# Kernel tuning notes

Hardware: AMD Instinct MI355X
Metric: run time of the kernel (lower is better)

The kernel has to match this reference:

```python
import jax, jax.numpy as jnp
import numpy as np

NUM_CLASSES = 80
L_BOX, L_OBJ, L_CLS = 5.0, 1.0, 1.0


def setup_inputs() -> dict:
    key = jax.random.key(0)
    k0, k1, k2, k3, k4 = jax.random.split(key, 5)
    B, N = 32, 50
    C = 5 + NUM_CLASSES
    pred0 = jax.random.normal(k0, (B, C, 64, 64), dtype=jnp.float32)
    pred1 = jax.random.normal(k1, (B, C, 32, 32), dtype=jnp.float32)
    pred2 = jax.random.normal(k2, (B, C, 16, 16), dtype=jnp.float32)
    # normalized cxcywh in (0,1)
    boxes = jax.random.uniform(k3, (B, N, 4), dtype=jnp.float32, minval=0.01, maxval=0.99)
    labels = jax.random.randint(k4, (B, N), 0, NUM_CLASSES, dtype=jnp.int32)
    return {"pred0": pred0, "pred1": pred1, "pred2": pred2, "boxes": boxes, "labels": labels}


def _bce_with_logits_mean(x, t):
    # numerically stable BCEWithLogits, mean reduction
    return jnp.mean(jnp.maximum(x, 0.0) - x * t + jnp.log1p(jnp.exp(-jnp.abs(x))))


def _build_targets(boxes, labels, b, h, w):
    # boxes: [B,N,4] normalized cxcywh; labels: [B,N]
    B, N, _ = boxes.shape
    bi = jnp.repeat(jnp.arange(B), N)            # [B*N]
    bf = boxes.reshape(-1, 4)                    # [B*N,4]
    lf = labels.reshape(-1)                      # [B*N]
    gx = bf[:, 0] * w
    gy = bf[:, 1] * h
    gi = jnp.minimum(gx.astype(jnp.int32), w - 1)  # int() truncation; gx >= 0
    gj = jnp.minimum(gy.astype(jnp.int32), h - 1)
    obj_t = jnp.zeros((b, 1, h, w), jnp.float32).at[bi, 0, gj, gi].set(1.0)
    vals = jnp.stack([gx - gi, gy - gj, bf[:, 2], bf[:, 3]], axis=1)  # [B*N,4]
    ch4 = jnp.arange(4)
    box_t = jnp.zeros((b, 4, h, w), jnp.float32).at[
        bi[:, None], ch4[None, :], gj[:, None], gi[:, None]].set(vals)
    cls_t = jnp.zeros((b, NUM_CLASSES, h, w), jnp.float32).at[bi, lf, gj, gi].set(1.0)
    return box_t, obj_t, cls_t


def _scale_loss(pred, boxes, labels):
    b, _, h, w = pred.shape
    box_t, obj_t, cls_t = _build_targets(boxes, labels, b, h, w)
    pb = jnp.clip(pred[:, :4], -10.0, 10.0)
    po = jnp.clip(pred[:, 4:5], -10.0, 10.0)
    pc = jnp.clip(pred[:, 5:], -10.0, 10.0)
    box_loss = jnp.mean((pb - box_t) ** 2)
    obj_loss = _bce_with_logits_mean(po, obj_t)
    cls_loss = _bce_with_logits_mean(pc, cls_t)
    # torch code zeroes non-finite losses; clamped logits keep these finite,
    # mirrored with jnp.where for faithfulness
    box_loss = jnp.where(jnp.isfinite(box_loss), box_loss, 0.0)
    obj_loss = jnp.where(jnp.isfinite(obj_loss), obj_loss, 0.0)
    cls_loss = jnp.where(jnp.isfinite(cls_loss), cls_loss, 0.0)
    return L_BOX * box_loss + L_OBJ * obj_loss + L_CLS * cls_loss


def reference(pred0, pred1, pred2, boxes, labels):
    total = (_scale_loss(pred0, boxes, labels)
             + _scale_loss(pred1, boxes, labels)
             + _scale_loss(pred2, boxes, labels))
    return jnp.clip(total / 3.0, 0.0, 1000000.0)
```

## Files before the change

kernel.cpp:

```cpp
#include <hip/hip_runtime.h>
#include <math.h>

#define NCLS 80
#define BB   32
#define NBOX 50
#define CC   85

#define GRID1 2048
#define BLK1  256

__device__ __forceinline__ float clip10(float x) {
    return fminf(fmaxf(x, -10.f), 10.f);
}

__device__ __forceinline__ float bce0(float x) {
    return fmaxf(x, 0.f) + __logf(1.f + __expf(-fabsf(x)));
}

__global__ __launch_bounds__(BLK1) void base_kernel(
    const float* __restrict__ p0, const float* __restrict__ p1,
    const float* __restrict__ p2, double* __restrict__ partial)
{
    const int tid = blockIdx.x * BLK1 + threadIdx.x;
    const int nth = GRID1 * BLK1;
    const float* ps[3] = {p0, p1, p2};
    const int hw4s[3]  = {64*64/4, 32*32/4, 16*16/4};

    float part[9];
    #pragma unroll
    for (int s = 0; s < 3; ++s) {
        const float4* p = (const float4*)ps[s];
        const int hw4 = hw4s[s];
        const int n4  = BB * CC * hw4;
        float bx = 0.f, ob = 0.f, cl = 0.f;
        for (int i = tid; i < n4; i += nth) {
            float4 v = p[i];
            int c = (i / hw4) % CC;
            float a0 = clip10(v.x), a1 = clip10(v.y);
            float a2 = clip10(v.z), a3 = clip10(v.w);
            if (c < 4) {
                bx += a0*a0 + a1*a1 + a2*a2 + a3*a3;
            } else if (c == 4) {
                ob += bce0(a0) + bce0(a1) + bce0(a2) + bce0(a3);
            } else {
                cl += bce0(a0) + bce0(a1) + bce0(a2) + bce0(a3);
            }
        }
        part[3*s+0] = bx; part[3*s+1] = ob; part[3*s+2] = cl;
    }

    #pragma unroll
    for (int k = 0; k < 9; ++k) {
        float v = part[k];
        #pragma unroll
        for (int off = 32; off > 0; off >>= 1) v += __shfl_down(v, off);
        part[k] = v;
    }
    __shared__ float sred[BLK1/64][9];
    const int wave = threadIdx.x >> 6;
    const int lane = threadIdx.x & 63;
    if (lane == 0) {
        #pragma unroll
        for (int k = 0; k < 9; ++k) sred[wave][k] = part[k];
    }
    __syncthreads();
    if (threadIdx.x == 0) {
        double* o = partial + (size_t)blockIdx.x * 9;
        #pragma unroll
        for (int k = 0; k < 9; ++k)
            o[k] = (double)(sred[0][k] + sred[1][k] + sred[2][k] + sred[3][k]);
    }
}

__global__ __launch_bounds__(64) void corr_kernel(
    const float* __restrict__ p0, const float* __restrict__ p1,
    const float* __restrict__ p2,
    const float* __restrict__ boxes, const int* __restrict__ labels,
    double* __restrict__ acc)
{
    const int s = blockIdx.x / BB;
    const int b = blockIdx.x % BB;
    const float* ps[3] = {p0, p1, p2};
    const int Ws[3] = {64, 32, 16};
    const int W = Ws[s], H = W, hw = W * W;
    const float* pred = ps[s];

    __shared__ int   s_cell[NBOX];
    __shared__ int   s_lab[NBOX];
    __shared__ float s_vx[NBOX], s_vy[NBOX], s_vw[NBOX], s_vh[NBOX];

    const int n = threadIdx.x;
    if (n < NBOX) {
        const float* bp = boxes + ((size_t)b * NBOX + n) * 4;
        float gx = bp[0] * (float)W;
        float gy = bp[1] * (float)H;
        int gi = min((int)gx, W - 1);
        int gj = min((int)gy, H - 1);
        s_cell[n] = gj * W + gi;
        s_lab[n]  = labels[b * NBOX + n];
        s_vx[n] = gx - (float)gi;
        s_vy[n] = gy - (float)gj;
        s_vw[n] = bp[2];
        s_vh[n] = bp[3];
    }
    __syncthreads();

    float cbx = 0.f, cob = 0.f, ccl = 0.f;
    if (n < NBOX) {
        const int cell = s_cell[n], lab = s_lab[n];
        bool lastCell = true, lastCls = true;
        for (int m = n + 1; m < NBOX; ++m) {
            if (s_cell[m] == cell) {
                lastCell = false;
                if (s_lab[m] == lab) lastCls = false;
            }
        }
        const float* pb_base = pred + (size_t)(b * CC) * hw + cell;
        if (lastCell) {
            float vals[4] = {s_vx[n], s_vy[n], s_vw[n], s_vh[n]};
            #pragma unroll
            for (int c = 0; c < 4; ++c) {
                float pb = clip10(pb_base[c * hw]);
                float d  = pb - vals[c];
                cbx += d * d - pb * pb;
            }
            float po = clip10(pb_base[4 * hw]);
            cob -= po;
        }
        if (lastCls) {
            float pc = clip10(pb_base[(5 + lab) * hw]);
            ccl -= pc;
        }
    }
    #pragma unroll
    for (int off = 32; off > 0; off >>= 1) {
        cbx += __shfl_down(cbx, off);
        cob += __shfl_down(cob, off);
        ccl += __shfl_down(ccl, off);
    }
    if (threadIdx.x == 0) {
        atomicAdd(&acc[3*s+0], (double)cbx);
        atomicAdd(&acc[3*s+1], (double)cob);
        atomicAdd(&acc[3*s+2], (double)ccl);
    }
}

__global__ __launch_bounds__(256) void final_kernel(
    const double* __restrict__ partial, const double* __restrict__ acc,
    float* __restrict__ out, int nb)
{
    double loc[9];
    #pragma unroll
    for (int k = 0; k < 9; ++k) loc[k] = 0.0;
    for (int i = threadIdx.x; i < nb; i += 256) {
        const double* row = partial + (size_t)i * 9;
        #pragma unroll
        for (int k = 0; k < 9; ++k) loc[k] += row[k];
    }
    __shared__ double sd[256];
    __shared__ double tot[9];
    for (int k = 0; k < 9; ++k) {
        sd[threadIdx.x] = loc[k];
        __syncthreads();
        for (int off = 128; off > 0; off >>= 1) {
            if (threadIdx.x < off) sd[threadIdx.x] += sd[threadIdx.x + off];
            __syncthreads();
        }
        if (threadIdx.x == 0) tot[k] = sd[0] + acc[k];
        __syncthreads();
    }
    if (threadIdx.x == 0) {
        const double hws[3] = {4096.0, 1024.0, 256.0};
        double total = 0.0;
        for (int s = 0; s < 3; ++s) {
            double hw  = hws[s];
            double box = tot[3*s+0] / (32.0 * 4.0 * hw);
            double ob  = tot[3*s+1] / (32.0 * hw);
            double cl  = tot[3*s+2] / (32.0 * 80.0 * hw);
            total += 5.0 * box + ob + cl;
        }
        total /= 3.0;
        total = fmin(fmax(total, 0.0), 1000000.0);
        out[0] = (float)total;
    }
}

extern "C" void kernel_launch(void* const* d_in, const int* in_sizes, int n_in,
                              void* d_out, int out_size, void* d_ws, size_t ws_size,
                              hipStream_t stream)
{
    const float* p0     = (const float*)d_in[0];
    const float* p1     = (const float*)d_in[1];
    const float* p2     = (const float*)d_in[2];
    const float* boxes  = (const float*)d_in[3];
    const int*   labels = (const int*)d_in[4];
    float* out = (float*)d_out;

    double* acc     = (double*)d_ws;
    double* partial = (double*)d_ws + 16;

    hipMemsetAsync(acc, 0, 9 * sizeof(double), stream);
    base_kernel<<<GRID1, BLK1, 0, stream>>>(p0, p1, p2, partial);
    corr_kernel<<<3 * BB, 64, 0, stream>>>(p0, p1, p2, boxes, labels, acc);
    final_kernel<<<1, 256, 0, stream>>>(partial, acc, out, GRID1);
}
```

Baseline: 119.9 us.

## Fold target-correction pass into base reduction kernel and drop memset

Result: faster. 102.5 us (-14.5%).

```diff
diff --git a/kernel.cpp b/kernel.cpp
--- a/kernel.cpp
+++ b/kernel.cpp
@@ -19,7 +19,9 @@
 
 __global__ __launch_bounds__(BLK1) void base_kernel(
     const float* __restrict__ p0, const float* __restrict__ p1,
-    const float* __restrict__ p2, double* __restrict__ partial)
+    const float* __restrict__ p2,
+    const float* __restrict__ boxes, const int* __restrict__ labels,
+    double* __restrict__ partial)
 {
     const int tid = blockIdx.x * BLK1 + threadIdx.x;
     const int nth = GRID1 * BLK1;
@@ -49,6 +51,77 @@
         part[3*s+0] = bx; part[3*s+1] = ob; part[3*s+2] = cl;
     }
 
+    __shared__ int   s_cell[NBOX];
+    __shared__ int   s_lab[NBOX];
+    __shared__ float s_vx[NBOX], s_vy[NBOX], s_vw[NBOX], s_vh[NBOX];
+
+    const bool doCorr = (blockIdx.x < 3 * BB);
+    const int  cs = blockIdx.x / BB;
+    const int  cb = blockIdx.x % BB;
+    const int  Ws[3] = {64, 32, 16};
+
+    if (doCorr && threadIdx.x < 64) {
+        const int n = threadIdx.x;
+        const int W = Ws[cs];
+        if (n < NBOX) {
+            const float* bp = boxes + ((size_t)cb * NBOX + n) * 4;
+            float gx = bp[0] * (float)W;
+            float gy = bp[1] * (float)W;
+            int gi = min((int)gx, W - 1);
+            int gj = min((int)gy, W - 1);
+            s_cell[n] = gj * W + gi;
+            s_lab[n]  = labels[cb * NBOX + n];
+            s_vx[n] = gx - (float)gi;
+            s_vy[n] = gy - (float)gj;
+            s_vw[n] = bp[2];
+            s_vh[n] = bp[3];
+        }
+    }
+    __syncthreads();
+    if (doCorr && threadIdx.x < 64) {
+        const int n = threadIdx.x;
+        const int W = Ws[cs], hw = W * W;
+        const float* pred = ps[cs];
+        float cbx = 0.f, cob = 0.f, ccl = 0.f;
+        if (n < NBOX) {
+            const int cell = s_cell[n], lab = s_lab[n];
+            bool lastCell = true, lastCls = true;
+            for (int m = n + 1; m < NBOX; ++m) {
+                if (s_cell[m] == cell) {
+                    lastCell = false;
+                    if (s_lab[m] == lab) lastCls = false;
+                }
+            }
+            const float* pb_base = pred + (size_t)(cb * CC) * hw + cell;
+            if (lastCell) {
+                float vals[4] = {s_vx[n], s_vy[n], s_vw[n], s_vh[n]};
+                #pragma unroll
+                for (int c = 0; c < 4; ++c) {
+                    float pb = clip10(pb_base[c * hw]);
+                    float d  = pb - vals[c];
+                    cbx += d * d - pb * pb;
+                }
+                float po = clip10(pb_base[4 * hw]);
+                cob -= po;
+            }
+            if (lastCls) {
+                float pc = clip10(pb_base[(5 + lab) * hw]);
+                ccl -= pc;
+            }
+        }
+        #pragma unroll
+        for (int off = 32; off > 0; off >>= 1) {
+            cbx += __shfl_down(cbx, off);
+            cob += __shfl_down(cob, off);
+            ccl += __shfl_down(ccl, off);
+        }
+        if (n == 0) {
+            part[3*cs+0] += cbx;
+            part[3*cs+1] += cob;
+            part[3*cs+2] += ccl;
+        }
+    }
+
     #pragma unroll
     for (int k = 0; k < 9; ++k) {
         float v = part[k];
@@ -72,82 +145,8 @@
     }
 }
 
-__global__ __launch_bounds__(64) void corr_kernel(
-    const float* __restrict__ p0, const float* __restrict__ p1,
-    const float* __restrict__ p2,
-    const float* __restrict__ boxes, const int* __restrict__ labels,
-    double* __restrict__ acc)
-{
-    const int s = blockIdx.x / BB;
-    const int b = blockIdx.x % BB;
-    const float* ps[3] = {p0, p1, p2};
-    const int Ws[3] = {64, 32, 16};
-    const int W = Ws[s], H = W, hw = W * W;
-    const float* pred = ps[s];
-
-    __shared__ int   s_cell[NBOX];
-    __shared__ int   s_lab[NBOX];
-    __shared__ float s_vx[NBOX], s_vy[NBOX], s_vw[NBOX], s_vh[NBOX];
-
-    const int n = threadIdx.x;
-    if (n < NBOX) {
-        const float* bp = boxes + ((size_t)b * NBOX + n) * 4;
-        float gx = bp[0] * (float)W;
-        float gy = bp[1] * (float)H;
-        int gi = min((int)gx, W - 1);
-        int gj = min((int)gy, H - 1);
-        s_cell[n] = gj * W + gi;
-        s_lab[n]  = labels[b * NBOX + n];
-        s_vx[n] = gx - (float)gi;
-        s_vy[n] = gy - (float)gj;
-        s_vw[n] = bp[2];
-        s_vh[n] = bp[3];
-    }
-    __syncthreads();
-
-    float cbx = 0.f, cob = 0.f, ccl = 0.f;
-    if (n < NBOX) {
-        const int cell = s_cell[n], lab = s_lab[n];
-        bool lastCell = true, lastCls = true;
-        for (int m = n + 1; m < NBOX; ++m) {
-            if (s_cell[m] == cell) {
-                lastCell = false;
-                if (s_lab[m] == lab) lastCls = false;
-            }
-        }
-        const float* pb_base = pred + (size_t)(b * CC) * hw + cell;
-        if (lastCell) {
-            float vals[4] = {s_vx[n], s_vy[n], s_vw[n], s_vh[n]};
-            #pragma unroll
-            for (int c = 0; c < 4; ++c) {
-                float pb = clip10(pb_base[c * hw]);
-                float d  = pb - vals[c];
-                cbx += d * d - pb * pb;
-            }
-            float po = clip10(pb_base[4 * hw]);
-            cob -= po;
-        }
-        if (lastCls) {
-            float pc = clip10(pb_base[(5 + lab) * hw]);
-            ccl -= pc;
-        }
-    }
-    #pragma unroll
-    for (int off = 32; off > 0; off >>= 1) {
-        cbx += __shfl_down(cbx, off);
-        cob += __shfl_down(cob, off);
-        ccl += __shfl_down(ccl, off);
-    }
-    if (threadIdx.x == 0) {
-        atomicAdd(&acc[3*s+0], (double)cbx);
-        atomicAdd(&acc[3*s+1], (double)cob);
-        atomicAdd(&acc[3*s+2], (double)ccl);
-    }
-}
-
 __global__ __launch_bounds__(256) void final_kernel(
-    const double* __restrict__ partial, const double* __restrict__ acc,
-    float* __restrict__ out, int nb)
+    const double* __restrict__ partial, float* __restrict__ out, int nb)
 {
     double loc[9];
     #pragma unroll
@@ -157,26 +156,33 @@
         #pragma unroll
         for (int k = 0; k < 9; ++k) loc[k] += row[k];
     }
-    __shared__ double sd[256];
-    __shared__ double tot[9];
+    #pragma unroll
     for (int k = 0; k < 9; ++k) {
-        sd[threadIdx.x] = loc[k];
-        __syncthreads();
-        for (int off = 128; off > 0; off >>= 1) {
-            if (threadIdx.x < off) sd[threadIdx.x] += sd[threadIdx.x + off];
-            __syncthreads();
-        }
-        if (threadIdx.x == 0) tot[k] = sd[0] + acc[k];
-        __syncthreads();
-    }
+        double v = loc[k];
+        #pragma unroll
+        for (int off = 32; off > 0; off >>= 1) v += __shfl_down(v, off);
+        loc[k] = v;
+    }
+    __shared__ double sred[4][9];
+    const int wave = threadIdx.x >> 6;
+    const int lane = threadIdx.x & 63;
+    if (lane == 0) {
+        #pragma unroll
+        for (int k = 0; k < 9; ++k) sred[wave][k] = loc[k];
+    }
+    __syncthreads();
     if (threadIdx.x == 0) {
         const double hws[3] = {4096.0, 1024.0, 256.0};
         double total = 0.0;
+        #pragma unroll
         for (int s = 0; s < 3; ++s) {
             double hw  = hws[s];
-            double box = tot[3*s+0] / (32.0 * 4.0 * hw);
-            double ob  = tot[3*s+1] / (32.0 * hw);
-            double cl  = tot[3*s+2] / (32.0 * 80.0 * hw);
+            double tb = sred[0][3*s+0] + sred[1][3*s+0] + sred[2][3*s+0] + sred[3][3*s+0];
+            double to = sred[0][3*s+1] + sred[1][3*s+1] + sred[2][3*s+1] + sred[3][3*s+1];
+            double tc = sred[0][3*s+2] + sred[1][3*s+2] + sred[2][3*s+2] + sred[3][3*s+2];
+            double box = tb / (32.0 * 4.0 * hw);
+            double ob  = to / (32.0 * hw);
+            double cl  = tc / (32.0 * 80.0 * hw);
             total += 5.0 * box + ob + cl;
         }
         total /= 3.0;
@@ -196,11 +202,8 @@
     const int*   labels = (const int*)d_in[4];
     float* out = (float*)d_out;
 
-    double* acc     = (double*)d_ws;
-    double* partial = (double*)d_ws + 16;
-
-    hipMemsetAsync(acc, 0, 9 * sizeof(double), stream);
-    base_kernel<<<GRID1, BLK1, 0, stream>>>(p0, p1, p2, partial);
-    corr_kernel<<<3 * BB, 64, 0, stream>>>(p0, p1, p2, boxes, labels, acc);
-    final_kernel<<<1, 256, 0, stream>>>(partial, acc, out, GRID1);
-}
+    double* partial = (double*)d_ws;
+
+    base_kernel<<<GRID1, BLK1, 0, stream>>>(p0, p1, p2, boxes, labels, partial);
+    final_kernel<<<1, 256, 0, stream>>>(partial, out, GRID1);
+}
```
